# Optimization experiments

Measured on AMD Instinct MI355X. Metric: run time of the kernel, lower is better.

Reference implementation:

```python
import jax, jax.numpy as jnp
import numpy as np

NUM_HEADS = 8
HEAD_DIM = 64  # embed_dim 512 / 8 heads


def setup_inputs() -> dict:
    key = jax.random.key(0)
    k1, k2, k3 = jax.random.split(key, 3)
    B, S, D = 2, 4096, 512
    # xavier-uniform-ish scales for faithfulness to init (values don't affect math)
    x = jax.random.normal(k1, (B, S, D), dtype=jnp.float32)
    qkv_w = jax.random.normal(k2, (3 * D, D), dtype=jnp.float32) * (1.0 / np.sqrt(D))
    qkv_b = jnp.zeros((3 * D,), dtype=jnp.float32)
    o_w = jax.random.normal(k3, (D, D), dtype=jnp.float32) * (1.0 / np.sqrt(D))
    o_b = jnp.zeros((D,), dtype=jnp.float32)
    return {"x": x, "qkv_w": qkv_w, "qkv_b": qkv_b, "o_w": o_w, "o_b": o_b}


def reference(x, qkv_w, qkv_b, o_w, o_b):
    B, S, D = x.shape
    H, hd = NUM_HEADS, HEAD_DIM
    # qkv projection: torch Linear is x @ W^T + b
    qkv = jnp.einsum('bsd,ed->bse', x, qkv_w) + qkv_b        # [B, S, 3D]
    qkv = qkv.reshape(B, S, H, 3 * hd).transpose(0, 2, 1, 3)  # [B, H, S, 3hd]
    q, k, v = jnp.split(qkv, 3, axis=-1)                      # each [B, H, S, hd]
    scale = 1.0 / jnp.sqrt(jnp.float32(hd))
    logits = jnp.einsum('bhqd,bhkd->bhqk', q, k) * scale      # [B, H, S, S]
    attn = jax.nn.softmax(logits, axis=-1)
    vals = jnp.einsum('bhqk,bhkd->bhqd', attn, v)             # [B, H, S, hd]
    vals = vals.transpose(0, 2, 1, 3).reshape(B, S, D)        # [B, S, D]
    o = jnp.einsum('bsd,ed->bse', vals, o_w) + o_b            # [B, S, D]
    return o
```

## Files before the change

### kernel.cpp

```cpp
#include <hip/hip_runtime.h>
#include <hip/hip_bf16.h>


typedef __attribute__((ext_vector_type(8)))  __bf16 bf16x8;
typedef __attribute__((ext_vector_type(2)))  __bf16 bf16x2;
typedef __attribute__((ext_vector_type(4))) float  f32x4;
typedef __attribute__((ext_vector_type(16))) float  f32x16;

__device__ __forceinline__ unsigned cvtpk(float a, float b) {
    bf16x2 t; t.x = (__bf16)a; t.y = (__bf16)b;
    union { bf16x2 v; unsigned u; } u; u.v = t; return u.u;
}
#if __has_builtin(__builtin_amdgcn_exp2f)
__device__ __forceinline__ float fexp2(float x) { return __builtin_amdgcn_exp2f(x); }
#else
__device__ __forceinline__ float fexp2(float x) { return exp2f(x); }
#endif
__device__ __forceinline__ void gload16(const unsigned short* g, unsigned short* l) {
    __builtin_amdgcn_global_load_lds(
        (const __attribute__((address_space(1))) void*)g,
        (__attribute__((address_space(3))) void*)l, 16, 0, 0);
}

__device__ __forceinline__ int swz(int row, int col) {
    return row * 64 + (col ^ ((row & 7) << 3));
}

__global__ __launch_bounds__(256) void qkv_gemm(
    const float* __restrict__ X, const float* __restrict__ W,
    const float* __restrict__ bias,
    unsigned short* __restrict__ Qb, unsigned short* __restrict__ Kb,
    unsigned short* __restrict__ Vtg)
{
    __shared__ __attribute__((aligned(16))) unsigned short SH[128 * 144];
    unsigned short* As = &SH[0];
    unsigned short* Bs = &SH[8192];
    const int tid = threadIdx.x;
    const int wid = tid >> 6, lane = tid & 63;
    const int hi = lane >> 4, lo = lane & 15;
    const int wm = wid >> 1, wn = wid & 1;
    const int m0 = blockIdx.x * 128;
    const bool isV = (blockIdx.y >= 8);
    const int b = m0 >> 12, sb = m0 & 4095;

    f32x4 acc[4][4] = {};

    if (!isV) {
        const int by3 = blockIdx.y & 3, tt = blockIdx.y >> 2;
        const float QSCL = 0.125f * 1.44269504088896f;
        const float sc = (tt == 0) ? QSCL : 1.0f;

        for (int k0 = 0; k0 < 512; k0 += 64) {
            __syncthreads();
            #pragma unroll
            for (int i = 0; i < 8; ++i) {
                const int c = i * 256 + tid;
                const int row = c >> 4, kc = (c & 15) << 2;
                const float4 va = *(const float4*)(X + (size_t)(m0 + row) * 512 + k0 + kc);
                uint2 pa; pa.x = cvtpk(va.x, va.y); pa.y = cvtpk(va.z, va.w);
                *(uint2*)&As[swz(row, kc)] = pa;
                const int nW = (by3 * 2 + (row >> 6)) * 192 + tt * 64 + (row & 63);
                const float4 vb = *(const float4*)(W + (size_t)nW * 512 + k0 + kc);
                uint2 pb; pb.x = cvtpk(vb.x, vb.y); pb.y = cvtpk(vb.z, vb.w);
                *(uint2*)&Bs[swz(row, kc)] = pb;
            }
            __syncthreads();
            #pragma unroll
            for (int ks = 0; ks < 2; ++ks) {
                bf16x8 af[4], bfr[4];
                #pragma unroll
                for (int mi = 0; mi < 4; ++mi)
                    af[mi] = *(const bf16x8*)&As[swz(wm * 64 + mi * 16 + lo, ks * 32 + hi * 8)];
                #pragma unroll
                for (int ni = 0; ni < 4; ++ni)
                    bfr[ni] = *(const bf16x8*)&Bs[swz(wn * 64 + ni * 16 + lo, ks * 32 + hi * 8)];
                #pragma unroll
                for (int mi = 0; mi < 4; ++mi)
                    #pragma unroll
                    for (int ni = 0; ni < 4; ++ni)
                        acc[mi][ni] = __builtin_amdgcn_mfma_f32_16x16x32_bf16(
                            bfr[ni], af[mi], acc[mi][ni], 0, 0, 0);
            }
        }
        __syncthreads();

        #pragma unroll
        for (int ni = 0; ni < 4; ++ni) {
            const int hq = by3 * 2 + wn;
            const float4 bv4 = *(const float4*)&bias[hq * 192 + tt * 64 + ni * 16 + hi * 4];
            #pragma unroll
            for (int mi = 0; mi < 4; ++mi) {
                const int srow_ = wm * 64 + mi * 16 + lo;
                uint2 w;
                w.x = cvtpk((acc[mi][ni][0] + bv4.x) * sc, (acc[mi][ni][1] + bv4.y) * sc);
                w.y = cvtpk((acc[mi][ni][2] + bv4.z) * sc, (acc[mi][ni][3] + bv4.w) * sc);
                *(uint2*)&SH[srow_ * 144 + wn * 72 + ni * 16 + hi * 4] = w;
            }
        }
        __syncthreads();

        unsigned short* dst = tt ? Kb : Qb;
        #pragma unroll
        for (int c = 0; c < 2; ++c) {
            const int h = by3 * 2 + c;
            #pragma unroll
            for (int qq = 0; qq < 4; ++qq) {
                const int slot = qq * 256 + tid;
                const int row = slot >> 3, g = slot & 7;
                const uint4 v = *(const uint4*)&SH[row * 144 + c * 72 + g * 8];
                *(uint4*)(dst + (((size_t)(b * 8 + h)) * 4096 + sb + row) * 64 + g * 8) = v;
            }
        }
    } else {
        const int by = blockIdx.y - 8;

        for (int k0 = 0; k0 < 512; k0 += 64) {
            __syncthreads();
            #pragma unroll
            for (int i = 0; i < 8; ++i) {
                const int c = i * 256 + tid;
                const int row = c >> 4, kc = (c & 15) << 2;
                const float4 va = *(const float4*)(X + (size_t)(m0 + row) * 512 + k0 + kc);
                uint2 pa; pa.x = cvtpk(va.x, va.y); pa.y = cvtpk(va.z, va.w);
                *(uint2*)&As[swz(row, kc)] = pa;
                const int nW = (by * 2 + (row >> 6)) * 192 + 128 + (row & 63);
                const float4 vb = *(const float4*)(W + (size_t)nW * 512 + k0 + kc);
                uint2 pb; pb.x = cvtpk(vb.x, vb.y); pb.y = cvtpk(vb.z, vb.w);
                *(uint2*)&Bs[swz(row, kc)] = pb;
            }
            __syncthreads();
            #pragma unroll
            for (int ks = 0; ks < 2; ++ks) {
                bf16x8 af[4], bfr[4];
                #pragma unroll
                for (int mi = 0; mi < 4; ++mi)
                    af[mi] = *(const bf16x8*)&As[swz(wm * 64 + mi * 16 + lo, ks * 32 + hi * 8)];
                #pragma unroll
                for (int ni = 0; ni < 4; ++ni)
                    bfr[ni] = *(const bf16x8*)&Bs[swz(wn * 64 + ni * 16 + lo, ks * 32 + hi * 8)];
                #pragma unroll
                for (int mi = 0; mi < 4; ++mi)
                    #pragma unroll
                    for (int ni = 0; ni < 4; ++ni)
                        acc[mi][ni] = __builtin_amdgcn_mfma_f32_16x16x32_bf16(
                            af[mi], bfr[ni], acc[mi][ni], 0, 0, 0);
            }
        }
        __syncthreads();

        #pragma unroll
        for (int ni = 0; ni < 4; ++ni) {
            const int d = ni * 16 + lo;
            const float bv = bias[(by * 2 + wn) * 192 + 128 + d];
            #pragma unroll
            for (int mi = 0; mi < 4; ++mi) {
                const int ml = wm * 64 + mi * 16 + hi * 4;
                uint2 w;
                w.x = cvtpk(acc[mi][ni][0] + bv, acc[mi][ni][1] + bv);
                w.y = cvtpk(acc[mi][ni][2] + bv, acc[mi][ni][3] + bv);
                *(uint2*)&SH[wn * 8704 + d * 136 + ml] = w;
            }
        }
        __syncthreads();

        #pragma unroll
        for (int qq = 0; qq < 8; ++qq) {
            const int slot = qq * 256 + tid;
            const int c = slot >> 10, d = (slot >> 4) & 63, mb = slot & 15;
            const int src = c * 8704 + d * 136 + 16 * (mb >> 1) + 4 * (mb & 1);
            const uint2 a  = *(const uint2*)&SH[src];
            const uint2 bb = *(const uint2*)&SH[src + 8];
            uint4 w; w.x = a.x; w.y = a.y; w.z = bb.x; w.w = bb.y;
            const int h = by * 2 + c;
            *(uint4*)(Vtg + ((size_t)((b * 8 + h) * 64 + d)) * 4096 + sb + 8 * mb) = w;
        }
    }
}

__global__ __launch_bounds__(512, 2) void attn_fwd(
    const unsigned short* __restrict__ Qb,
    const unsigned short* __restrict__ Kb,
    const unsigned short* __restrict__ Vtg,
    unsigned short* __restrict__ Ob)
{
    __shared__ __attribute__((aligned(16))) unsigned short smem[2][4][2][4096];

    const int tid = threadIdx.x;
    const int wid = tid >> 6, lane = tid & 63;
    const int l31 = lane & 31, hl = lane >> 5;
    const int n_ = blockIdx.x;
    const int bh = (n_ & 7) * 2 + ((n_ >> 3) & 1);
    const int qb = n_ >> 4;
    const int b = bh >> 3, h = bh & 7;
    const int q0 = qb * 256 + wid * 32;
    const size_t kbase = (size_t)bh * 4096 * 64;
    const size_t vbase = (size_t)bh * 64 * 4096;

    const int srow = tid >> 3;
    const int sg = (tid & 7) ^ (srow & 7);
    const unsigned short* kS = Kb + kbase + (size_t)srow * 64 + sg * 8;
    const unsigned short* vS = Vtg + vbase + (size_t)srow * 4096 + sg * 8;

    bf16x8 qf[4];
    #pragma unroll
    for (int dk = 0; dk < 4; ++dk)
        qf[dk] = *(const bf16x8*)(Qb + kbase + (size_t)(q0 + l31) * 64 + dk * 16 + hl * 8);

    f32x16 o0 = {}, o1 = {};
    float l_run = 0.0f;

    const int s7 = l31 & 7;
    const int baseA = l31 * 64, baseB = (32 + l31) * 64;
    const int ldst = tid * 8;

    #pragma unroll
    for (int i = 0; i < 4; ++i) {
        gload16(kS + (size_t)i * 4096, &smem[0][i][0][ldst]);
        gload16(vS + (size_t)i * 64,   &smem[0][i][1][ldst]);
    }
    asm volatile("s_waitcnt vmcnt(0)" ::: "memory");
    __builtin_amdgcn_s_barrier();
    __builtin_amdgcn_sched_barrier(0);

    for (int g = 0; g < 16; ++g) {
        const int cur = g & 1;
        if (g < 15) {
            #pragma unroll
            for (int i = 0; i < 4; ++i) {
                const size_t T = 4 * (g + 1) + i;
                gload16(kS + T * 4096, &smem[cur ^ 1][i][0][ldst]);
                gload16(vS + T * 64,   &smem[cur ^ 1][i][1][ldst]);
            }
        }
        #pragma unroll
        for (int ti = 0; ti < 4; ++ti) {
            const unsigned short* KT = &smem[cur][ti][0][0];
            const unsigned short* VT = &smem[cur][ti][1][0];

            f32x16 s0 = {}, s1 = {};
            __builtin_amdgcn_s_setprio(1);
            #pragma unroll
            for (int dk = 0; dk < 4; ++dk) {
                const int gk = dk * 2 + hl;
                const bf16x8 kA = *(const bf16x8*)(KT + baseA + 8 * (gk ^ s7));
                const bf16x8 kB = *(const bf16x8*)(KT + baseB + 8 * (gk ^ s7));
                s0 = __builtin_amdgcn_mfma_f32_32x32x16_bf16(kA, qf[dk], s0, 0, 0, 0);
                s1 = __builtin_amdgcn_mfma_f32_32x32x16_bf16(kB, qf[dk], s1, 0, 0, 0);
            }
            __builtin_amdgcn_s_setprio(0);

            #pragma unroll
            for (int i = 0; i < 16; ++i) {
                s0[i] = fexp2(s0[i]);
                s1[i] = fexp2(s1[i]);
            }
            float lsA = 0.f, lsB = 0.f, lsC = 0.f, lsD = 0.f;
            #pragma unroll
            for (int i = 0; i < 4; ++i) {
                lsA += s0[i];      lsB += s0[i + 4];
                lsA += s0[i + 8];  lsB += s0[i + 12];
                lsC += s1[i];      lsD += s1[i + 4];
                lsC += s1[i + 8];  lsD += s1[i + 12];
            }
            l_run += (lsA + lsB) + (lsC + lsD);

            union U8 { unsigned u[4]; bf16x8 v; };
            U8 p0, p1, p2, p3;
            #pragma unroll
            for (int i = 0; i < 4; ++i) {
                p0.u[i] = cvtpk(s0[2 * i],     s0[2 * i + 1]);
                p1.u[i] = cvtpk(s0[2 * i + 8], s0[2 * i + 9]);
                p2.u[i] = cvtpk(s1[2 * i],     s1[2 * i + 1]);
                p3.u[i] = cvtpk(s1[2 * i + 8], s1[2 * i + 9]);
            }
            const bf16x8 pf[4] = { p0.v, p1.v, p2.v, p3.v };

            __builtin_amdgcn_s_setprio(1);
            #pragma unroll
            for (int ks = 0; ks < 4; ++ks) {
                const int gv = ((2 * ks + hl) ^ s7) << 3;
                const bf16x8 va = *(const bf16x8*)(VT + baseA + gv);
                const bf16x8 vb = *(const bf16x8*)(VT + baseB + gv);
                o0 = __builtin_amdgcn_mfma_f32_32x32x16_bf16(va, pf[ks], o0, 0, 0, 0);
                o1 = __builtin_amdgcn_mfma_f32_32x32x16_bf16(vb, pf[ks], o1, 0, 0, 0);
            }
            __builtin_amdgcn_s_setprio(0);
        }
        asm volatile("s_waitcnt vmcnt(0)" ::: "memory");
        __builtin_amdgcn_s_barrier();
        __builtin_amdgcn_sched_barrier(0);
    }

    l_run += __shfl_xor(l_run, 32);
    unsigned short* Ew = &smem[0][0][0][0] + wid * 2048;
    const int prow = l31 * 64;
    const float inv = 1.0f / l_run;
    #pragma unroll
    for (int u = 0; u < 4; ++u) {
        uint2 w0, w1;
        w0.x = cvtpk(o0[4 * u] * inv, o0[4 * u + 1] * inv);
        w0.y = cvtpk(o0[4 * u + 2] * inv, o0[4 * u + 3] * inv);
        *(uint2*)&Ew[prow + ((u ^ s7) << 3) + (hl << 2)] = w0;
        w1.x = cvtpk(o1[4 * u] * inv, o1[4 * u + 1] * inv);
        w1.y = cvtpk(o1[4 * u + 2] * inv, o1[4 * u + 3] * inv);
        *(uint2*)&Ew[prow + (((4 + u) ^ s7) << 3) + (hl << 2)] = w1;
    }
    asm volatile("s_waitcnt lgkmcnt(0)" ::: "memory");
    __builtin_amdgcn_sched_barrier(0);
    #pragma unroll
    for (int rr = 0; rr < 4; ++rr) {
        const int qrow = (lane >> 3) + rr * 8;
        const int gphys = (lane & 7) ^ (qrow & 7);
        const uint4 v = *(const uint4*)&Ew[qrow * 64 + gphys * 8];
        *(uint4*)(Ob + ((size_t)b * 4096 + q0 + qrow) * 512 + h * 64 + (lane & 7) * 8) = v;
    }
}

__global__ __launch_bounds__(256) void oproj_gemm(
    const unsigned short* __restrict__ A, const float* __restrict__ W,
    const float* __restrict__ bias, float* __restrict__ C)
{
    __shared__ __attribute__((aligned(16))) unsigned short As[128 * 64];
    __shared__ __attribute__((aligned(16))) unsigned short Bs[128 * 64];
    const int tid = threadIdx.x;
    const int wid = tid >> 6, lane = tid & 63;
    const int hi = lane >> 4, lo = lane & 15;
    const int wm = wid >> 1, wn = wid & 1;
    const int m0 = blockIdx.x * 128, n0 = blockIdx.y * 128;

    f32x4 acc[4][4] = {};
    for (int k0 = 0; k0 < 512; k0 += 64) {
        __syncthreads();
        #pragma unroll
        for (int i = 0; i < 4; ++i) {
            const int c = i * 256 + tid;
            const int row = c >> 3, kc = (c & 7) << 3;
            *(uint4*)&As[swz(row, kc)] =
                *(const uint4*)(A + (size_t)(m0 + row) * 512 + k0 + kc);
        }
        #pragma unroll
        for (int i = 0; i < 8; ++i) {
            const int c = i * 256 + tid;
            const int row = c >> 4, kc = (c & 15) << 2;
            const float4 vb = *(const float4*)(W + (size_t)(n0 + row) * 512 + k0 + kc);
            uint2 pb; pb.x = cvtpk(vb.x, vb.y); pb.y = cvtpk(vb.z, vb.w);
            *(uint2*)&Bs[swz(row, kc)] = pb;
        }
        __syncthreads();
        #pragma unroll
        for (int ks = 0; ks < 2; ++ks) {
            bf16x8 af[4], bfr[4];
            #pragma unroll
            for (int mi = 0; mi < 4; ++mi)
                af[mi] = *(const bf16x8*)&As[swz(wm * 64 + mi * 16 + lo, ks * 32 + hi * 8)];
            #pragma unroll
            for (int ni = 0; ni < 4; ++ni)
                bfr[ni] = *(const bf16x8*)&Bs[swz(wn * 64 + ni * 16 + lo, ks * 32 + hi * 8)];
            #pragma unroll
            for (int mi = 0; mi < 4; ++mi)
                #pragma unroll
                for (int ni = 0; ni < 4; ++ni)
                    acc[mi][ni] = __builtin_amdgcn_mfma_f32_16x16x32_bf16(
                        af[mi], bfr[ni], acc[mi][ni], 0, 0, 0);
        }
    }

    #pragma unroll
    for (int mi = 0; mi < 4; ++mi) {
        #pragma unroll
        for (int ni = 0; ni < 4; ++ni) {
            const int n = n0 + wn * 64 + ni * 16 + lo;
            const float bv = bias[n];
            #pragma unroll
            for (int j = 0; j < 4; ++j) {
                const int m = m0 + wm * 64 + mi * 16 + hi * 4 + j;
                C[(size_t)m * 512 + n] = acc[mi][ni][j] + bv;
            }
        }
    }
}

extern "C" void kernel_launch(void* const* d_in, const int* in_sizes, int n_in,
                              void* d_out, int out_size, void* d_ws, size_t ws_size,
                              hipStream_t stream) {
    const float* x     = (const float*)d_in[0];
    const float* qkv_w = (const float*)d_in[1];
    const float* qkv_b = (const float*)d_in[2];
    const float* o_w   = (const float*)d_in[3];
    const float* o_b   = (const float*)d_in[4];
    float* out = (float*)d_out;

    const size_t NELEM = (size_t)2 * 8 * 4096 * 64;
    unsigned short* Qb  = (unsigned short*)d_ws;
    unsigned short* Kb  = Qb + NELEM;
    unsigned short* Vtg = Kb + NELEM;
    unsigned short* Ob  = Vtg + NELEM;

    qkv_gemm<<<dim3(64, 12), 256, 0, stream>>>(x, qkv_w, qkv_b, Qb, Kb, Vtg);
    attn_fwd<<<dim3(256), 512, 0, stream>>>(Qb, Kb, Vtg, Ob);
    oproj_gemm<<<dim3(64, 4), 256, 0, stream>>>(Ob, o_w, o_b, out);
}
```

Before: 120.8 us.

## Pre-convert inputs to bf16 and stage GEMM tiles via direct global-to-LDS loads

A new pre-pass kernel converts x, qkv_w and o_w from fp32 to bf16 into workspace. The QKV and output-projection GEMMs then load tiles with global_load_lds into swizzled LDS instead of loading fp32 through registers and converting inside every block, which removes redundant conversion work and halves the bytes fetched per tile. The attention kernel also drops its s_setprio hints and splits the PV accumulators into two chains per output to shorten MFMA dependency chains. The cost is an extra launch, an extra pass over x, and the attention output buffer now aliases the converted-x buffer.

```diff
diff --git a/kernel.cpp b/kernel.cpp
--- a/kernel.cpp
+++ b/kernel.cpp
@@ -26,8 +26,27 @@
     return row * 64 + (col ^ ((row & 7) << 3));
 }
 
+__global__ __launch_bounds__(256) void cvt_bf16(
+    const float* __restrict__ X, const float* __restrict__ Wq,
+    const float* __restrict__ Ow,
+    unsigned short* __restrict__ Xb, unsigned short* __restrict__ Wqb,
+    unsigned short* __restrict__ Owb)
+{
+    int c = blockIdx.x * 256 + threadIdx.x;
+    const float* src; unsigned short* dst;
+    if (c < 524288)      { src = X  + (size_t)c * 8; dst = Xb  + (size_t)c * 8; }
+    else if (c < 622592) { c -= 524288; src = Wq + (size_t)c * 8; dst = Wqb + (size_t)c * 8; }
+    else                 { c -= 622592; src = Ow + (size_t)c * 8; dst = Owb + (size_t)c * 8; }
+    const float4 a = ((const float4*)src)[0];
+    const float4 b = ((const float4*)src)[1];
+    uint4 w;
+    w.x = cvtpk(a.x, a.y); w.y = cvtpk(a.z, a.w);
+    w.z = cvtpk(b.x, b.y); w.w = cvtpk(b.z, b.w);
+    *(uint4*)dst = w;
+}
+
 __global__ __launch_bounds__(256) void qkv_gemm(
-    const float* __restrict__ X, const float* __restrict__ W,
+    const unsigned short* __restrict__ Xb, const unsigned short* __restrict__ Wqb,
     const float* __restrict__ bias,
     unsigned short* __restrict__ Qb, unsigned short* __restrict__ Kb,
     unsigned short* __restrict__ Vtg)
@@ -43,47 +62,64 @@
     const bool isV = (blockIdx.y >= 8);
     const int b = m0 >> 12, sb = m0 & 4095;
 
+    const int sg = (tid & 7) ^ ((tid >> 3) & 7);
+    const unsigned short* xS = Xb + (size_t)(m0 + (tid >> 3)) * 512 + sg * 8;
+    const unsigned short* wS[4];
+    {
+        const int by3 = blockIdx.y & 3, tt = blockIdx.y >> 2;
+        const int byv = blockIdx.y - 8;
+        #pragma unroll
+        for (int i = 0; i < 4; ++i) {
+            const int row = i * 32 + (tid >> 3);
+            const int nW = isV ? (byv * 2 + (row >> 6)) * 192 + 128 + (row & 63)
+                               : (by3 * 2 + (row >> 6)) * 192 + tt * 64 + (row & 63);
+            wS[i] = Wqb + (size_t)nW * 512 + sg * 8;
+        }
+    }
+
     f32x4 acc[4][4] = {};
 
-    if (!isV) {
-        const int by3 = blockIdx.y & 3, tt = blockIdx.y >> 2;
-        const float QSCL = 0.125f * 1.44269504088896f;
-        const float sc = (tt == 0) ? QSCL : 1.0f;
-
-        for (int k0 = 0; k0 < 512; k0 += 64) {
-            __syncthreads();
-            #pragma unroll
-            for (int i = 0; i < 8; ++i) {
-                const int c = i * 256 + tid;
-                const int row = c >> 4, kc = (c & 15) << 2;
-                const float4 va = *(const float4*)(X + (size_t)(m0 + row) * 512 + k0 + kc);
-                uint2 pa; pa.x = cvtpk(va.x, va.y); pa.y = cvtpk(va.z, va.w);
-                *(uint2*)&As[swz(row, kc)] = pa;
-                const int nW = (by3 * 2 + (row >> 6)) * 192 + tt * 64 + (row & 63);
-                const float4 vb = *(const float4*)(W + (size_t)nW * 512 + k0 + kc);
-                uint2 pb; pb.x = cvtpk(vb.x, vb.y); pb.y = cvtpk(vb.z, vb.w);
-                *(uint2*)&Bs[swz(row, kc)] = pb;
-            }
-            __syncthreads();
-            #pragma unroll
-            for (int ks = 0; ks < 2; ++ks) {
-                bf16x8 af[4], bfr[4];
-                #pragma unroll
-                for (int mi = 0; mi < 4; ++mi)
-                    af[mi] = *(const bf16x8*)&As[swz(wm * 64 + mi * 16 + lo, ks * 32 + hi * 8)];
-                #pragma unroll
-                for (int ni = 0; ni < 4; ++ni)
-                    bfr[ni] = *(const bf16x8*)&Bs[swz(wn * 64 + ni * 16 + lo, ks * 32 + hi * 8)];
+    for (int k0 = 0; k0 < 512; k0 += 64) {
+        __syncthreads();
+        #pragma unroll
+        for (int i = 0; i < 4; ++i) {
+            gload16(xS + i * 16384 + k0, &As[(i * 256 + tid) * 8]);
+            gload16(wS[i] + k0, &Bs[(i * 256 + tid) * 8]);
+        }
+        asm volatile("s_waitcnt vmcnt(0)" ::: "memory");
+        __syncthreads();
+        #pragma unroll
+        for (int ks = 0; ks < 2; ++ks) {
+            bf16x8 af[4], bfr[4];
+            #pragma unroll
+            for (int mi = 0; mi < 4; ++mi)
+                af[mi] = *(const bf16x8*)&As[swz(wm * 64 + mi * 16 + lo, ks * 32 + hi * 8)];
+            #pragma unroll
+            for (int ni = 0; ni < 4; ++ni)
+                bfr[ni] = *(const bf16x8*)&Bs[swz(wn * 64 + ni * 16 + lo, ks * 32 + hi * 8)];
+            if (!isV) {
                 #pragma unroll
                 for (int mi = 0; mi < 4; ++mi)
                     #pragma unroll
                     for (int ni = 0; ni < 4; ++ni)
                         acc[mi][ni] = __builtin_amdgcn_mfma_f32_16x16x32_bf16(
                             bfr[ni], af[mi], acc[mi][ni], 0, 0, 0);
-            }
-        }
-        __syncthreads();
-
+            } else {
+                #pragma unroll
+                for (int mi = 0; mi < 4; ++mi)
+                    #pragma unroll
+                    for (int ni = 0; ni < 4; ++ni)
+                        acc[mi][ni] = __builtin_amdgcn_mfma_f32_16x16x32_bf16(
+                            af[mi], bfr[ni], acc[mi][ni], 0, 0, 0);
+            }
+        }
+    }
+    __syncthreads();
+
+    if (!isV) {
+        const int by3 = blockIdx.y & 3, tt = blockIdx.y >> 2;
+        const float QSCL = 0.125f * 1.44269504088896f;
+        const float sc = (tt == 0) ? QSCL : 1.0f;
         #pragma unroll
         for (int ni = 0; ni < 4; ++ni) {
             const int hq = by3 * 2 + wn;
@@ -98,7 +134,6 @@
             }
         }
         __syncthreads();
-
         unsigned short* dst = tt ? Kb : Qb;
         #pragma unroll
         for (int c = 0; c < 2; ++c) {
@@ -113,41 +148,6 @@
         }
     } else {
         const int by = blockIdx.y - 8;
-
-        for (int k0 = 0; k0 < 512; k0 += 64) {
-            __syncthreads();
-            #pragma unroll
-            for (int i = 0; i < 8; ++i) {
-                const int c = i * 256 + tid;
-                const int row = c >> 4, kc = (c & 15) << 2;
-                const float4 va = *(const float4*)(X + (size_t)(m0 + row) * 512 + k0 + kc);
-                uint2 pa; pa.x = cvtpk(va.x, va.y); pa.y = cvtpk(va.z, va.w);
-                *(uint2*)&As[swz(row, kc)] = pa;
-                const int nW = (by * 2 + (row >> 6)) * 192 + 128 + (row & 63);
-                const float4 vb = *(const float4*)(W + (size_t)nW * 512 + k0 + kc);
-                uint2 pb; pb.x = cvtpk(vb.x, vb.y); pb.y = cvtpk(vb.z, vb.w);
-                *(uint2*)&Bs[swz(row, kc)] = pb;
-            }
-            __syncthreads();
-            #pragma unroll
-            for (int ks = 0; ks < 2; ++ks) {
-                bf16x8 af[4], bfr[4];
-                #pragma unroll
-                for (int mi = 0; mi < 4; ++mi)
-                    af[mi] = *(const bf16x8*)&As[swz(wm * 64 + mi * 16 + lo, ks * 32 + hi * 8)];
-                #pragma unroll
-                for (int ni = 0; ni < 4; ++ni)
-                    bfr[ni] = *(const bf16x8*)&Bs[swz(wn * 64 + ni * 16 + lo, ks * 32 + hi * 8)];
-                #pragma unroll
-                for (int mi = 0; mi < 4; ++mi)
-                    #pragma unroll
-                    for (int ni = 0; ni < 4; ++ni)
-                        acc[mi][ni] = __builtin_amdgcn_mfma_f32_16x16x32_bf16(
-                            af[mi], bfr[ni], acc[mi][ni], 0, 0, 0);
-            }
-        }
-        __syncthreads();
-
         #pragma unroll
         for (int ni = 0; ni < 4; ++ni) {
             const int d = ni * 16 + lo;
@@ -162,7 +162,6 @@
             }
         }
         __syncthreads();
-
         #pragma unroll
         for (int qq = 0; qq < 8; ++qq) {
             const int slot = qq * 256 + tid;
@@ -206,7 +205,7 @@
     for (int dk = 0; dk < 4; ++dk)
         qf[dk] = *(const bf16x8*)(Qb + kbase + (size_t)(q0 + l31) * 64 + dk * 16 + hl * 8);
 
-    f32x16 o0 = {}, o1 = {};
+    f32x16 o0a = {}, o0b = {}, o1a = {}, o1b = {};
     float l_run = 0.0f;
 
     const int s7 = l31 & 7;
@@ -238,7 +237,6 @@
             const unsigned short* VT = &smem[cur][ti][1][0];
 
             f32x16 s0 = {}, s1 = {};
-            __builtin_amdgcn_s_setprio(1);
             #pragma unroll
             for (int dk = 0; dk < 4; ++dk) {
                 const int gk = dk * 2 + hl;
@@ -247,7 +245,6 @@
                 s0 = __builtin_amdgcn_mfma_f32_32x32x16_bf16(kA, qf[dk], s0, 0, 0, 0);
                 s1 = __builtin_amdgcn_mfma_f32_32x32x16_bf16(kB, qf[dk], s1, 0, 0, 0);
             }
-            __builtin_amdgcn_s_setprio(0);
 
             #pragma unroll
             for (int i = 0; i < 16; ++i) {
@@ -275,22 +272,26 @@
             }
             const bf16x8 pf[4] = { p0.v, p1.v, p2.v, p3.v };
 
-            __builtin_amdgcn_s_setprio(1);
             #pragma unroll
             for (int ks = 0; ks < 4; ++ks) {
                 const int gv = ((2 * ks + hl) ^ s7) << 3;
                 const bf16x8 va = *(const bf16x8*)(VT + baseA + gv);
                 const bf16x8 vb = *(const bf16x8*)(VT + baseB + gv);
-                o0 = __builtin_amdgcn_mfma_f32_32x32x16_bf16(va, pf[ks], o0, 0, 0, 0);
-                o1 = __builtin_amdgcn_mfma_f32_32x32x16_bf16(vb, pf[ks], o1, 0, 0, 0);
-            }
-            __builtin_amdgcn_s_setprio(0);
+                if (ks & 1) {
+                    o0b = __builtin_amdgcn_mfma_f32_32x32x16_bf16(va, pf[ks], o0b, 0, 0, 0);
+                    o1b = __builtin_amdgcn_mfma_f32_32x32x16_bf16(vb, pf[ks], o1b, 0, 0, 0);
+                } else {
+                    o0a = __builtin_amdgcn_mfma_f32_32x32x16_bf16(va, pf[ks], o0a, 0, 0, 0);
+                    o1a = __builtin_amdgcn_mfma_f32_32x32x16_bf16(vb, pf[ks], o1a, 0, 0, 0);
+                }
+            }
         }
         asm volatile("s_waitcnt vmcnt(0)" ::: "memory");
         __builtin_amdgcn_s_barrier();
         __builtin_amdgcn_sched_barrier(0);
     }
 
+    f32x16 o0 = o0a + o0b, o1 = o1a + o1b;
     l_run += __shfl_xor(l_run, 32);
     unsigned short* Ew = &smem[0][0][0][0] + wid * 2048;
     const int prow = l31 * 64;
@@ -317,7 +318,7 @@
 }
 
 __global__ __launch_bounds__(256) void oproj_gemm(
-    const unsigned short* __restrict__ A, const float* __restrict__ W,
+    const unsigned short* __restrict__ A, const unsigned short* __restrict__ Wb,
     const float* __restrict__ bias, float* __restrict__ C)
 {
     __shared__ __attribute__((aligned(16))) unsigned short As[128 * 64];
@@ -328,24 +329,19 @@
     const int wm = wid >> 1, wn = wid & 1;
     const int m0 = blockIdx.x * 128, n0 = blockIdx.y * 128;
 
+    const int sg = (tid & 7) ^ ((tid >> 3) & 7);
+    const unsigned short* aS = A  + (size_t)(m0 + (tid >> 3)) * 512 + sg * 8;
+    const unsigned short* bS = Wb + (size_t)(n0 + (tid >> 3)) * 512 + sg * 8;
+
     f32x4 acc[4][4] = {};
     for (int k0 = 0; k0 < 512; k0 += 64) {
         __syncthreads();
         #pragma unroll
         for (int i = 0; i < 4; ++i) {
-            const int c = i * 256 + tid;
-            const int row = c >> 3, kc = (c & 7) << 3;
-            *(uint4*)&As[swz(row, kc)] =
-                *(const uint4*)(A + (size_t)(m0 + row) * 512 + k0 + kc);
-        }
-        #pragma unroll
-        for (int i = 0; i < 8; ++i) {
-            const int c = i * 256 + tid;
-            const int row = c >> 4, kc = (c & 15) << 2;
-            const float4 vb = *(const float4*)(W + (size_t)(n0 + row) * 512 + k0 + kc);
-            uint2 pb; pb.x = cvtpk(vb.x, vb.y); pb.y = cvtpk(vb.z, vb.w);
-            *(uint2*)&Bs[swz(row, kc)] = pb;
-        }
+            gload16(aS + i * 16384 + k0, &As[(i * 256 + tid) * 8]);
+            gload16(bS + i * 16384 + k0, &Bs[(i * 256 + tid) * 8]);
+        }
+        asm volatile("s_waitcnt vmcnt(0)" ::: "memory");
         __syncthreads();
         #pragma unroll
         for (int ks = 0; ks < 2; ++ks) {
@@ -394,9 +390,12 @@
     unsigned short* Qb  = (unsigned short*)d_ws;
     unsigned short* Kb  = Qb + NELEM;
     unsigned short* Vtg = Kb + NELEM;
-    unsigned short* Ob  = Vtg + NELEM;
-
-    qkv_gemm<<<dim3(64, 12), 256, 0, stream>>>(x, qkv_w, qkv_b, Qb, Kb, Vtg);
-    attn_fwd<<<dim3(256), 512, 0, stream>>>(Qb, Kb, Vtg, Ob);
-    oproj_gemm<<<dim3(64, 4), 256, 0, stream>>>(Ob, o_w, o_b, out);
-}
+    unsigned short* ObXb = Vtg + NELEM;
+    unsigned short* Wqb = ObXb + NELEM;
+    unsigned short* Owb = Wqb + 786432;
+
+    cvt_bf16<<<dim3(2560), 256, 0, stream>>>(x, qkv_w, o_w, ObXb, Wqb, Owb);
+    qkv_gemm<<<dim3(64, 12), 256, 0, stream>>>(ObXb, Wqb, qkv_b, Qb, Kb, Vtg);
+    attn_fwd<<<dim3(256), 512, 0, stream>>>(Qb, Kb, Vtg, ObXb);
+    oproj_gemm<<<dim3(64, 4), 256, 0, stream>>>(ObXb, Owb, o_b, out);
+}
```

Result: no change. 121.5 us (+0.6%).
